# Optimization experiments

Hardware: AMD Instinct MI355X
Metric: run time of the kernel (lower is better)

## Reference

```python
import jax, jax.numpy as jnp
import numpy as np

B, T, L = 16, 32, 128
D = 768            # PhoBERT-base hidden size
NH = 12            # attn_num_heads
HD = D // NH
VOCAB = 64000
NEG = -1e9


def setup_inputs() -> dict:
    key = jax.random.key(0)
    ks = jax.random.split(key, 12)
    input_ids = jax.random.randint(ks[0], (B, T, L), 0, VOCAB, dtype=jnp.int32)
    attention_mask = jnp.ones((B, T, L), dtype=jnp.float32)
    # ragged number of real turns per dialogue
    num_turns = jax.random.randint(ks[1], (B,), 4, T + 1)
    turn_mask = (jnp.arange(T)[None, :] < num_turns[:, None]).astype(jnp.float32)
    s = 0.02
    embed = jax.random.normal(ks[2], (VOCAB, D), jnp.float32) * s
    Wq = jax.random.normal(ks[3], (D, D), jnp.float32) * s
    Wk = jax.random.normal(ks[4], (D, D), jnp.float32) * s
    Wv = jax.random.normal(ks[5], (D, D), jnp.float32) * s
    Wo = jax.random.normal(ks[6], (D, D), jnp.float32) * s
    bq = jnp.zeros((D,), jnp.float32)
    bk = jnp.zeros((D,), jnp.float32)
    bv = jnp.zeros((D,), jnp.float32)
    bo = jnp.zeros((D,), jnp.float32)
    Wh = jax.random.normal(ks[7], (2 * D,), jnp.float32) * s
    bh = jnp.zeros((), jnp.float32)
    return dict(input_ids=input_ids, attention_mask=attention_mask,
                turn_mask=turn_mask, embed=embed,
                Wq=Wq, bq=bq, Wk=Wk, bk=bk, Wv=Wv, bv=bv, Wo=Wo, bo=bo,
                Wh=Wh, bh=bh)


def _forward(input_ids, attention_mask, turn_mask, embed,
             Wq, bq, Wk, bk, Wv, bv, Wo, bo, Wh, bh):
    # --- turn encoder (frozen PhoBERT stand-in): embedding + masked mean pool ---
    emb = embed[input_ids]                                  # [B,T,L,D]
    m = attention_mask[..., None]                           # [B,T,L,1]
    H = (emb * m).sum(axis=2) / jnp.clip(m.sum(axis=2), 1.0)  # [B,T,D]

    # --- cross-turn attention: query = h_t, keys/values = H[:t] (strictly causal) ---
    q = (H @ Wq + bq).reshape(B, T, NH, HD)
    k = (H @ Wk + bk).reshape(B, T, NH, HD)
    v = (H @ Wv + bv).reshape(B, T, NH, HD)
    scores = jnp.einsum('bqhd,bkhd->bhqk', q, k) / np.sqrt(HD)  # [B,NH,T,T]
    idx = jnp.arange(T)
    strict = (idx[None, :, None] > idx[None, None, :])          # [1,T,T] j < i
    kmask = strict & (turn_mask[:, None, :] > 0)                # [B,T,T]
    scores = jnp.where(kmask[:, None, :, :], scores, NEG)
    attn = jax.nn.softmax(scores, axis=-1)
    ctx = jnp.einsum('bhqk,bkhd->bqhd', attn, v).reshape(B, T, D)
    ctx = ctx @ Wo + bo                                         # [B,T,D]
    # t == 0 uses c_t = zeros (no MHA output, no output bias)
    ctx = ctx * (idx > 0)[None, :, None]

    # --- evidence head + noisy-or recurrence ---
    z = jnp.concatenate([H, ctx], axis=-1)                      # [B,T,2D]
    s = z @ Wh + bh                                             # [B,T]
    qprob = jax.nn.sigmoid(s) * turn_mask                       # padded turns -> q=0
    one_minus = 1.0 - qprob
    p_agg = 1.0 - jnp.cumprod(one_minus, axis=1)                # [B,T]
    p_dialogue = 1.0 - jnp.prod(one_minus, axis=1)              # [B]
    return qprob, p_agg, p_dialogue


def reference(input_ids, attention_mask, turn_mask, embed,
              Wq, bq, Wk, bk, Wv, bv, Wo, bo, Wh, bh):
    return _forward(input_ids, attention_mask, turn_mask, embed,
                    Wq, bq, Wk, bk, Wv, bv, Wo, bo, Wh, bh)
```

## Files before the change

### kernel.cpp

```cpp
#include <hip/hip_runtime.h>
#include <hip/hip_bf16.h>
#include <math.h>

#define B_ 16
#define T_ 32
#define L_ 128
#define D_ 768
#define NH_ 12
#define HD_ 64
#define M_ (B_*T_)

typedef __attribute__((ext_vector_type(8))) short s16x8;
typedef __attribute__((ext_vector_type(4))) float f32x4;
typedef __attribute__((ext_vector_type(8))) unsigned short u16x8;

__device__ __forceinline__ unsigned short f2bf(float x) {
    unsigned int b = __float_as_uint(x);
    b += 0x7FFFu + ((b >> 16) & 1u);
    return (unsigned short)(b >> 16);
}

#define MFMA16(a, b, c) __builtin_amdgcn_mfma_f32_16x16x32_bf16(a, b, c, 0, 0, 0)

__global__ __launch_bounds__(384) void pool_prep_kernel(
    const int* __restrict__ ids, const float* __restrict__ amask,
    const float* __restrict__ embed,
    const float* __restrict__ Wq, const float* __restrict__ Wk,
    const float* __restrict__ Wv, const float* __restrict__ Wo,
    unsigned short* __restrict__ Wt, unsigned short* __restrict__ Wot,
    float* __restrict__ Ppart, float* __restrict__ PartM)
{
    const int bx  = blockIdx.x;
    const int tid = threadIdx.x;
    if (bx < M_*4) {
        const int bt = bx >> 2, l0 = (bx & 3) * 32;
        const int tx = tid % 96, ph = tid / 96;
        __shared__ int   sid[32];
        __shared__ float smk[32];
        __shared__ float red[4][96][9];
        if (tid < 32) {
            sid[tid] = ids[bt*L_ + l0 + tid];
            smk[tid] = amask[bt*L_ + l0 + tid];
        }
        __syncthreads();
        float a0=0,a1=0,a2=0,a3=0,a4=0,a5=0,a6=0,a7=0, msump=0.f;
        #pragma unroll 8
        for (int l = ph; l < 32; l += 4) {
            float m = smk[l];
            msump += m;
            const float4* p = (const float4*)(embed + (size_t)sid[l]*D_) + (tx << 1);
            float4 v0 = p[0], v1 = p[1];
            a0 = fmaf(v0.x, m, a0); a1 = fmaf(v0.y, m, a1);
            a2 = fmaf(v0.z, m, a2); a3 = fmaf(v0.w, m, a3);
            a4 = fmaf(v1.x, m, a4); a5 = fmaf(v1.y, m, a5);
            a6 = fmaf(v1.z, m, a6); a7 = fmaf(v1.w, m, a7);
        }
        float* rr = red[ph][tx];
        rr[0]=a0; rr[1]=a1; rr[2]=a2; rr[3]=a3; rr[4]=a4; rr[5]=a5; rr[6]=a6; rr[7]=a7;
        if (tx == 0) rr[8] = msump;
        __syncthreads();
        if (ph == 0) {
            float4 o0, o1;
            o0.x = red[0][tx][0]+red[1][tx][0]+red[2][tx][0]+red[3][tx][0];
            o0.y = red[0][tx][1]+red[1][tx][1]+red[2][tx][1]+red[3][tx][1];
            o0.z = red[0][tx][2]+red[1][tx][2]+red[2][tx][2]+red[3][tx][2];
            o0.w = red[0][tx][3]+red[1][tx][3]+red[2][tx][3]+red[3][tx][3];
            o1.x = red[0][tx][4]+red[1][tx][4]+red[2][tx][4]+red[3][tx][4];
            o1.y = red[0][tx][5]+red[1][tx][5]+red[2][tx][5]+red[3][tx][5];
            o1.z = red[0][tx][6]+red[1][tx][6]+red[2][tx][6]+red[3][tx][6];
            o1.w = red[0][tx][7]+red[1][tx][7]+red[2][tx][7]+red[3][tx][7];
            float* dst = Ppart + (size_t)bx*D_ + tx*8;
            *(float4*)dst = o0;
            *(float4*)(dst + 4) = o1;
            if (tx == 0)
                PartM[bx] = red[0][0][8]+red[1][0][8]+red[2][0][8]+red[3][0][8];
        }
    } else {
        const int idx = bx - M_*4;
        const int z   = idx / 384;
        const int rem = idx % 384;
        const int n0  = (rem % 16) * 48;
        const int k0  = (rem / 16) * 32;
        const float* __restrict__ W = (z==0)?Wq:(z==1)?Wk:(z==2)?Wv:Wo;
        unsigned short* __restrict__ outp = (z<3) ? (Wt + (size_t)z*D_*D_) : Wot;
        __shared__ float tile[32][49];
        {
            const int tx2 = tid % 48, ty2 = tid / 48;
            #pragma unroll
            for (int r = 0; r < 4; ++r)
                tile[ty2 + r*8][tx2] = W[(size_t)(k0 + ty2 + r*8)*D_ + n0 + tx2];
        }
        __syncthreads();
        {
            const int tk = tid % 32, tn = tid / 32;
            #pragma unroll
            for (int r = 0; r < 4; ++r)
                outp[(size_t)(n0 + tn + r*12)*D_ + k0 + tk] = f2bf(tile[tk][tn + r*12]);
        }
    }
}

__global__ __launch_bounds__(96) void combine_kernel(
    const float* __restrict__ Ppart, const float* __restrict__ PartM,
    const float* __restrict__ Wh,
    unsigned short* __restrict__ Hbf, float* __restrict__ s1)
{
    const int bt = blockIdx.x, tx = threadIdx.x;
    __shared__ float dp[96];
    float msum = PartM[bt*4] + PartM[bt*4+1] + PartM[bt*4+2] + PartM[bt*4+3];
    float inv = 1.f / fmaxf(msum, 1.f);
    const float* p0 = Ppart + (size_t)(bt*4)*D_ + tx*8;
    float s[8];
    #pragma unroll
    for (int k = 0; k < 8; ++k)
        s[k] = (p0[k] + p0[D_ + k] + p0[2*D_ + k] + p0[3*D_ + k]) * inv;
    u16x8 hb;
    #pragma unroll
    for (int k = 0; k < 8; ++k) hb[k] = f2bf(s[k]);
    *(u16x8*)(Hbf + (size_t)bt*D_ + tx*8) = hb;
    float d = 0.f;
    #pragma unroll
    for (int k = 0; k < 8; ++k) d = fmaf(s[k], Wh[tx*8 + k], d);
    dp[tx] = d;
    __syncthreads();
    if (tx < 32) {
        float dd = dp[tx] + dp[tx+32] + dp[tx+64];
        #pragma unroll
        for (int off = 16; off > 0; off >>= 1) dd += __shfl_xor(dd, off, 32);
        if (tx == 0) s1[bt] = dd;
    }
}

__global__ __launch_bounds__(256) void qkv_attn_kernel(
    const unsigned short* __restrict__ Hbf,
    const unsigned short* __restrict__ Wt,
    const float* __restrict__ bq, const float* __restrict__ bk, const float* __restrict__ bv,
    const float* __restrict__ tmask,
    unsigned short* __restrict__ ctx)
{
    const int b = blockIdx.x / NH_;
    const int h = blockIdx.x % NH_;
    const int tid  = threadIdx.x;
    const int lane = tid & 63;
    const int w    = tid >> 6;
    const int r16  = lane & 15;
    const int kgrp = lane >> 4;

    __shared__ unsigned short Hs[32][776];
    __shared__ unsigned short Qs[32][72];
    __shared__ unsigned short Ks[32][72];
    __shared__ unsigned short Vt[64][40];
    __shared__ unsigned short Ps[32][40];

    const unsigned short* hsrc = Hbf + (size_t)b*T_*D_;
    #pragma unroll
    for (int it = 0; it < 12; ++it) {
        int e = it*256 + tid;
        int row = e / 96, cg = e % 96;
        *(s16x8*)&Hs[row][cg*8] = *(const s16x8*)(hsrc + row*D_ + cg*8);
    }
    __syncthreads();

    const int nc = h*HD_ + w*16 + r16;
    const unsigned short* wq = Wt + (size_t)nc*D_;
    const unsigned short* wk = wq + (size_t)D_*D_;
    const unsigned short* wv = wk + (size_t)D_*D_;
    f32x4 aQ0={0,0,0,0},aQ1={0,0,0,0},aK0={0,0,0,0},aK1={0,0,0,0},aV0={0,0,0,0},aV1={0,0,0,0};
    s16x8 pq = *(const s16x8*)(wq + kgrp*8);
    s16x8 pk = *(const s16x8*)(wk + kgrp*8);
    s16x8 pv = *(const s16x8*)(wv + kgrp*8);
    for (int k0 = 0; k0 < D_; k0 += 32) {
        s16x8 cq = pq, ck = pk, cv = pv;
        int kn = k0 + 32;
        if (kn < D_) {
            pq = *(const s16x8*)(wq + kn + kgrp*8);
            pk = *(const s16x8*)(wk + kn + kgrp*8);
            pv = *(const s16x8*)(wv + kn + kgrp*8);
        }
        s16x8 a0 = *(const s16x8*)&Hs[r16][k0 + kgrp*8];
        s16x8 a1 = *(const s16x8*)&Hs[16 + r16][k0 + kgrp*8];
        aQ0 = MFMA16(a0, cq, aQ0); aQ1 = MFMA16(a1, cq, aQ1);
        aK0 = MFMA16(a0, ck, aK0); aK1 = MFMA16(a1, ck, aK1);
        aV0 = MFMA16(a0, cv, aV0); aV1 = MFMA16(a1, cv, aV1);
    }
    {
        const int c = w*16 + r16;
        const float bQ = bq[h*HD_ + c], bK = bk[h*HD_ + c], bV = bv[h*HD_ + c];
        #pragma unroll
        for (int mi = 0; mi < 2; ++mi) {
            f32x4 q_ = mi ? aQ1 : aQ0;
            f32x4 k_ = mi ? aK1 : aK0;
            f32x4 v_ = mi ? aV1 : aV0;
            #pragma unroll
            for (int r = 0; r < 4; ++r) {
                int i = mi*16 + kgrp*4 + r;
                Qs[i][c] = f2bf(q_[r] + bQ);
                Ks[i][c] = f2bf(k_[r] + bK);
                Vt[c][i] = f2bf(v_[r] + bV);
            }
        }
    }
    __syncthreads();

    f32x4 s00={0,0,0,0}, s01={0,0,0,0}, s10={0,0,0,0}, s11={0,0,0,0};
    #pragma unroll
    for (int ks = 0; ks < 2; ++ks) {
        s16x8 q0 = *(const s16x8*)&Qs[r16][ks*32 + kgrp*8];
        s16x8 q1 = *(const s16x8*)&Qs[16 + r16][ks*32 + kgrp*8];
        s16x8 k0v = *(const s16x8*)&Ks[r16][ks*32 + kgrp*8];
        s16x8 k1v = *(const s16x8*)&Ks[16 + r16][ks*32 + kgrp*8];
        s00 = MFMA16(q0, k0v, s00); s01 = MFMA16(q0, k1v, s01);
        s10 = MFMA16(q1, k0v, s10); s11 = MFMA16(q1, k1v, s11);
    }

    const float tmj0 = tmask[b*T_ + r16];
    const float tmj1 = tmask[b*T_ + 16 + r16];
    const int miW = w >> 1, niW = w & 1;
    #pragma unroll
    for (int mi = 0; mi < 2; ++mi) {
        f32x4 sv0 = mi ? s10 : s00;
        f32x4 sv1 = mi ? s11 : s01;
        #pragma unroll
        for (int r = 0; r < 4; ++r) {
            int i = mi*16 + kgrp*4 + r;
            float v0 = (r16 < i      && tmj0 > 0.f) ? sv0[r]*0.125f : -1e9f;
            float v1 = (16 + r16 < i && tmj1 > 0.f) ? sv1[r]*0.125f : -1e9f;
            float mx = fmaxf(v0, v1);
            #pragma unroll
            for (int off = 1; off < 16; off <<= 1) mx = fmaxf(mx, __shfl_xor(mx, off));
            float e0 = __expf(v0 - mx), e1 = __expf(v1 - mx);
            float sm = e0 + e1;
            #pragma unroll
            for (int off = 1; off < 16; off <<= 1) sm += __shfl_xor(sm, off);
            float inv = 1.f / sm;
            if (mi == miW) {
                float p = (niW ? e1 : e0) * inv;
                Ps[i][niW*16 + r16] = f2bf(p);
            }
        }
    }
    __syncthreads();

    {
        s16x8 ap0 = *(const s16x8*)&Ps[r16][kgrp*8];
        s16x8 ap1 = *(const s16x8*)&Ps[16 + r16][kgrp*8];
        s16x8 bvv = *(const s16x8*)&Vt[w*16 + r16][kgrp*8];
        f32x4 o0 = {0,0,0,0}, o1 = {0,0,0,0};
        o0 = MFMA16(ap0, bvv, o0);
        o1 = MFMA16(ap1, bvv, o1);
        #pragma unroll
        for (int mi = 0; mi < 2; ++mi) {
            f32x4 o_ = mi ? o1 : o0;
            #pragma unroll
            for (int r = 0; r < 4; ++r) {
                int i = mi*16 + kgrp*4 + r;
                ctx[(size_t)(b*T_ + i)*D_ + h*HD_ + w*16 + r16] = f2bf(o_[r]);
            }
        }
    }
}

__global__ __launch_bounds__(256) void gemm_head_kernel(
    const unsigned short* __restrict__ Abf,
    const unsigned short* __restrict__ Wtn,
    const float* __restrict__ bias,
    const float* __restrict__ Wh,
    float* __restrict__ s2p)
{
    const int bn = blockIdx.x;
    const int n0 = bn * 64;
    const int m0 = blockIdx.y * 64;

    __shared__ unsigned short As[64][40];
    __shared__ unsigned short Bs[64][40];
    __shared__ float s2l[64][2];

    const int tid  = threadIdx.x;
    const int lane = tid & 63;
    const int wave = tid >> 6;
    const int wm   = wave >> 1;
    const int wn   = wave & 1;
    const int kgrp = lane >> 4;
    const int r16  = lane & 15;

    const int srow = tid >> 2;
    const int scol = (tid & 3) * 8;

    f32x4 acc00 = {0,0,0,0}, acc01 = {0,0,0,0}, acc10 = {0,0,0,0}, acc11 = {0,0,0,0};

    for (int k0 = 0; k0 < D_; k0 += 32) {
        s16x8 av = *(const s16x8*)(Abf + (size_t)(m0 + srow)*D_ + k0 + scol);
        s16x8 bv = *(const s16x8*)(Wtn + (size_t)(n0 + srow)*D_ + k0 + scol);
        *(s16x8*)&As[srow][scol] = av;
        *(s16x8*)&Bs[srow][scol] = bv;
        __syncthreads();
        s16x8 a0 = *(const s16x8*)&As[wm*32 +      r16][kgrp*8];
        s16x8 a1 = *(const s16x8*)&As[wm*32 + 16 + r16][kgrp*8];
        s16x8 bb0 = *(const s16x8*)&Bs[wn*32 +      r16][kgrp*8];
        s16x8 bb1 = *(const s16x8*)&Bs[wn*32 + 16 + r16][kgrp*8];
        acc00 = MFMA16(a0, bb0, acc00);
        acc01 = MFMA16(a0, bb1, acc01);
        acc10 = MFMA16(a1, bb0, acc10);
        acc11 = MFMA16(a1, bb1, acc11);
        __syncthreads();
    }

    float rp[2][4] = {};
    #pragma unroll
    for (int ni = 0; ni < 2; ++ni) {
        int col = n0 + wn*32 + ni*16 + r16;
        float w2 = Wh[D_ + col];
        float bv_ = bias[col];
        #pragma unroll
        for (int mi = 0; mi < 2; ++mi) {
            f32x4 c = (mi == 0) ? (ni == 0 ? acc00 : acc01) : (ni == 0 ? acc10 : acc11);
            #pragma unroll
            for (int r = 0; r < 4; ++r) {
                int m = m0 + wm*32 + mi*16 + kgrp*4 + r;
                float v = c[r] + bv_;
                if ((m & (T_ - 1)) == 0) v = 0.f;
                rp[mi][r] = fmaf(v, w2, rp[mi][r]);
            }
        }
    }
    #pragma unroll
    for (int mi = 0; mi < 2; ++mi)
        #pragma unroll
        for (int r = 0; r < 4; ++r) {
            float v = rp[mi][r];
            v += __shfl_xor(v, 1); v += __shfl_xor(v, 2);
            v += __shfl_xor(v, 4); v += __shfl_xor(v, 8);
            rp[mi][r] = v;
        }
    if (r16 == 0) {
        #pragma unroll
        for (int mi = 0; mi < 2; ++mi)
            #pragma unroll
            for (int r = 0; r < 4; ++r)
                s2l[wm*32 + mi*16 + kgrp*4 + r][wn] = rp[mi][r];
    }
    __syncthreads();
    if (tid < 64)
        s2p[(size_t)(m0 + tid)*12 + bn] = s2l[tid][0] + s2l[tid][1];
}

__global__ __launch_bounds__(512) void scan_kernel(
    const float* __restrict__ s1, const float* __restrict__ s2p,
    const float* __restrict__ bh, const float* __restrict__ tmask,
    float* __restrict__ qprob, float* __restrict__ p_agg, float* __restrict__ p_dlg)
{
    const int bt = threadIdx.x;
    const int t  = bt & 31, b = bt >> 5;
    float s = s1[bt] + bh[0];
    #pragma unroll
    for (int c = 0; c < 12; ++c) s += s2p[bt*12 + c];
    float q = (1.f / (1.f + __expf(-s))) * tmask[bt];
    qprob[bt] = q;
    float x = 1.f - q;
    #pragma unroll
    for (int off = 1; off < 32; off <<= 1) {
        float y = __shfl_up(x, off, 32);
        if (t >= off) x *= y;
    }
    p_agg[bt] = 1.f - x;
    if (t == 31) p_dlg[b] = 1.f - x;
}

extern "C" void kernel_launch(void* const* d_in, const int* in_sizes, int n_in,
                              void* d_out, int out_size, void* d_ws, size_t ws_size,
                              hipStream_t stream) {
    const int*   ids   = (const int*)  d_in[0];
    const float* amask = (const float*)d_in[1];
    const float* tmask = (const float*)d_in[2];
    const float* embed = (const float*)d_in[3];
    const float* Wq    = (const float*)d_in[4];
    const float* bq    = (const float*)d_in[5];
    const float* Wk    = (const float*)d_in[6];
    const float* bk    = (const float*)d_in[7];
    const float* Wv    = (const float*)d_in[8];
    const float* bv    = (const float*)d_in[9];
    const float* Wo    = (const float*)d_in[10];
    const float* bo    = (const float*)d_in[11];
    const float* Wh    = (const float*)d_in[12];
    const float* bh    = (const float*)d_in[13];
    float* out = (float*)d_out;

    unsigned short* Hbf   = (unsigned short*)d_ws;
    unsigned short* CTXbf = Hbf + (size_t)M_*D_;
    unsigned short* Wt    = CTXbf + (size_t)M_*D_;
    unsigned short* Wot   = Wt + (size_t)3*D_*D_;
    float* s1    = (float*)(Wot + (size_t)D_*D_);
    float* s2p   = s1 + M_;
    float* PartM = s2p + M_*12;
    float* Ppart = PartM + M_*4;

    pool_prep_kernel<<<M_*4 + 1536, 384, 0, stream>>>(
        ids, amask, embed, Wq, Wk, Wv, Wo, Wt, Wot, Ppart, PartM);
    combine_kernel<<<M_, 96, 0, stream>>>(Ppart, PartM, Wh, Hbf, s1);
    qkv_attn_kernel<<<B_*NH_, 256, 0, stream>>>(Hbf, Wt, bq, bk, bv, tmask, CTXbf);
    gemm_head_kernel<<<dim3(12, 8), 256, 0, stream>>>(CTXbf, Wot, bo, Wh, s2p);
    scan_kernel<<<1, 512, 0, stream>>>(s1, s2p, bh, tmask, out, out + M_, out + 2*M_);
}
```

Measured before the change: 66.85 us.

## Fuse pool/combine and gemm/scan kernels, prefetch GEMM tiles into registers

The pooling kernel now processes a whole turn per block, computing the mean, the bf16 H and the first head dot product in one pass. This removes the separate combine kernel and the partial-sum buffers. The scan is folded into the output GEMM through a last-block-done atomic counter per row tile, which removes another launch. The GEMM also prefetches the next K slice into registers while the current one is consumed. In exchange, the pooling stage has fewer, longer blocks (512 instead of 2048), which may reduce parallelism on the gather.

```diff
diff --git a/kernel.cpp b/kernel.cpp
--- a/kernel.cpp
+++ b/kernel.cpp
@@ -27,25 +27,30 @@
     const float* __restrict__ embed,
     const float* __restrict__ Wq, const float* __restrict__ Wk,
     const float* __restrict__ Wv, const float* __restrict__ Wo,
+    const float* __restrict__ Wh,
     unsigned short* __restrict__ Wt, unsigned short* __restrict__ Wot,
-    float* __restrict__ Ppart, float* __restrict__ PartM)
+    unsigned short* __restrict__ Hbf, float* __restrict__ s1,
+    int* __restrict__ cnt)
 {
     const int bx  = blockIdx.x;
     const int tid = threadIdx.x;
-    if (bx < M_*4) {
-        const int bt = bx >> 2, l0 = (bx & 3) * 32;
+    if (bx < M_) {
+        const int bt = bx;
         const int tx = tid % 96, ph = tid / 96;
-        __shared__ int   sid[32];
-        __shared__ float smk[32];
+        __shared__ int   sid[L_];
+        __shared__ float smk[L_];
         __shared__ float red[4][96][9];
-        if (tid < 32) {
-            sid[tid] = ids[bt*L_ + l0 + tid];
-            smk[tid] = amask[bt*L_ + l0 + tid];
+        __shared__ float dp[96];
+        if (tid < L_) {
+            sid[tid] = ids[bt*L_ + tid];
+            smk[tid] = amask[bt*L_ + tid];
+        } else if (bx == 0 && tid < L_ + 8) {
+            cnt[tid - L_] = 0;
         }
         __syncthreads();
         float a0=0,a1=0,a2=0,a3=0,a4=0,a5=0,a6=0,a7=0, msump=0.f;
         #pragma unroll 8
-        for (int l = ph; l < 32; l += 4) {
+        for (int l = ph; l < L_; l += 4) {
             float m = smk[l];
             msump += m;
             const float4* p = (const float4*)(embed + (size_t)sid[l]*D_) + (tx << 1);
@@ -60,23 +65,30 @@
         if (tx == 0) rr[8] = msump;
         __syncthreads();
         if (ph == 0) {
-            float4 o0, o1;
-            o0.x = red[0][tx][0]+red[1][tx][0]+red[2][tx][0]+red[3][tx][0];
-            o0.y = red[0][tx][1]+red[1][tx][1]+red[2][tx][1]+red[3][tx][1];
-            o0.z = red[0][tx][2]+red[1][tx][2]+red[2][tx][2]+red[3][tx][2];
-            o0.w = red[0][tx][3]+red[1][tx][3]+red[2][tx][3]+red[3][tx][3];
-            o1.x = red[0][tx][4]+red[1][tx][4]+red[2][tx][4]+red[3][tx][4];
-            o1.y = red[0][tx][5]+red[1][tx][5]+red[2][tx][5]+red[3][tx][5];
-            o1.z = red[0][tx][6]+red[1][tx][6]+red[2][tx][6]+red[3][tx][6];
-            o1.w = red[0][tx][7]+red[1][tx][7]+red[2][tx][7]+red[3][tx][7];
-            float* dst = Ppart + (size_t)bx*D_ + tx*8;
-            *(float4*)dst = o0;
-            *(float4*)(dst + 4) = o1;
-            if (tx == 0)
-                PartM[bx] = red[0][0][8]+red[1][0][8]+red[2][0][8]+red[3][0][8];
+            float msum = red[0][0][8]+red[1][0][8]+red[2][0][8]+red[3][0][8];
+            float inv = 1.f / fmaxf(msum, 1.f);
+            float s[8];
+            u16x8 hb;
+            #pragma unroll
+            for (int k = 0; k < 8; ++k) {
+                s[k] = (red[0][tx][k]+red[1][tx][k]+red[2][tx][k]+red[3][tx][k]) * inv;
+                hb[k] = f2bf(s[k]);
+            }
+            *(u16x8*)(Hbf + (size_t)bt*D_ + tx*8) = hb;
+            float d = 0.f;
+            #pragma unroll
+            for (int k = 0; k < 8; ++k) d = fmaf(s[k], Wh[tx*8 + k], d);
+            dp[tx] = d;
+        }
+        __syncthreads();
+        if (tid < 32) {
+            float dd = dp[tid] + dp[tid+32] + dp[tid+64];
+            #pragma unroll
+            for (int off = 16; off > 0; off >>= 1) dd += __shfl_xor(dd, off, 32);
+            if (tid == 0) s1[bt] = dd;
         }
     } else {
-        const int idx = bx - M_*4;
+        const int idx = bx - M_;
         const int z   = idx / 384;
         const int rem = idx % 384;
         const int n0  = (rem % 16) * 48;
@@ -97,37 +109,6 @@
             for (int r = 0; r < 4; ++r)
                 outp[(size_t)(n0 + tn + r*12)*D_ + k0 + tk] = f2bf(tile[tk][tn + r*12]);
         }
-    }
-}
-
-__global__ __launch_bounds__(96) void combine_kernel(
-    const float* __restrict__ Ppart, const float* __restrict__ PartM,
-    const float* __restrict__ Wh,
-    unsigned short* __restrict__ Hbf, float* __restrict__ s1)
-{
-    const int bt = blockIdx.x, tx = threadIdx.x;
-    __shared__ float dp[96];
-    float msum = PartM[bt*4] + PartM[bt*4+1] + PartM[bt*4+2] + PartM[bt*4+3];
-    float inv = 1.f / fmaxf(msum, 1.f);
-    const float* p0 = Ppart + (size_t)(bt*4)*D_ + tx*8;
-    float s[8];
-    #pragma unroll
-    for (int k = 0; k < 8; ++k)
-        s[k] = (p0[k] + p0[D_ + k] + p0[2*D_ + k] + p0[3*D_ + k]) * inv;
-    u16x8 hb;
-    #pragma unroll
-    for (int k = 0; k < 8; ++k) hb[k] = f2bf(s[k]);
-    *(u16x8*)(Hbf + (size_t)bt*D_ + tx*8) = hb;
-    float d = 0.f;
-    #pragma unroll
-    for (int k = 0; k < 8; ++k) d = fmaf(s[k], Wh[tx*8 + k], d);
-    dp[tx] = d;
-    __syncthreads();
-    if (tx < 32) {
-        float dd = dp[tx] + dp[tx+32] + dp[tx+64];
-        #pragma unroll
-        for (int off = 16; off > 0; off >>= 1) dd += __shfl_xor(dd, off, 32);
-        if (tx == 0) s1[bt] = dd;
     }
 }
 
@@ -260,12 +241,17 @@
     }
 }
 
-__global__ __launch_bounds__(256) void gemm_head_kernel(
+__global__ __launch_bounds__(256) void gemm_head_scan_kernel(
     const unsigned short* __restrict__ Abf,
     const unsigned short* __restrict__ Wtn,
     const float* __restrict__ bias,
     const float* __restrict__ Wh,
-    float* __restrict__ s2p)
+    const float* __restrict__ s1,
+    const float* __restrict__ bh,
+    const float* __restrict__ tmask,
+    int* __restrict__ cnt,
+    float* __restrict__ s2p,
+    float* __restrict__ qprob, float* __restrict__ p_agg, float* __restrict__ p_dlg)
 {
     const int bn = blockIdx.x;
     const int n0 = bn * 64;
@@ -274,6 +260,7 @@
     __shared__ unsigned short As[64][40];
     __shared__ unsigned short Bs[64][40];
     __shared__ float s2l[64][2];
+    __shared__ int sdone;
 
     const int tid  = threadIdx.x;
     const int lane = tid & 63;
@@ -288,12 +275,19 @@
 
     f32x4 acc00 = {0,0,0,0}, acc01 = {0,0,0,0}, acc10 = {0,0,0,0}, acc11 = {0,0,0,0};
 
+    const unsigned short* aptr = Abf + (size_t)(m0 + srow)*D_ + scol;
+    const unsigned short* bptr = Wtn + (size_t)(n0 + srow)*D_ + scol;
+    s16x8 av = *(const s16x8*)aptr;
+    s16x8 bv2 = *(const s16x8*)bptr;
+
     for (int k0 = 0; k0 < D_; k0 += 32) {
-        s16x8 av = *(const s16x8*)(Abf + (size_t)(m0 + srow)*D_ + k0 + scol);
-        s16x8 bv = *(const s16x8*)(Wtn + (size_t)(n0 + srow)*D_ + k0 + scol);
         *(s16x8*)&As[srow][scol] = av;
-        *(s16x8*)&Bs[srow][scol] = bv;
-        __syncthreads();
+        *(s16x8*)&Bs[srow][scol] = bv2;
+        __syncthreads();
+        if (k0 + 32 < D_) {
+            av  = *(const s16x8*)(aptr + k0 + 32);
+            bv2 = *(const s16x8*)(bptr + k0 + 32);
+        }
         s16x8 a0 = *(const s16x8*)&As[wm*32 +      r16][kgrp*8];
         s16x8 a1 = *(const s16x8*)&As[wm*32 + 16 + r16][kgrp*8];
         s16x8 bb0 = *(const s16x8*)&Bs[wn*32 +      r16][kgrp*8];
@@ -342,28 +336,32 @@
     __syncthreads();
     if (tid < 64)
         s2p[(size_t)(m0 + tid)*12 + bn] = s2l[tid][0] + s2l[tid][1];
-}
-
-__global__ __launch_bounds__(512) void scan_kernel(
-    const float* __restrict__ s1, const float* __restrict__ s2p,
-    const float* __restrict__ bh, const float* __restrict__ tmask,
-    float* __restrict__ qprob, float* __restrict__ p_agg, float* __restrict__ p_dlg)
-{
-    const int bt = threadIdx.x;
-    const int t  = bt & 31, b = bt >> 5;
-    float s = s1[bt] + bh[0];
-    #pragma unroll
-    for (int c = 0; c < 12; ++c) s += s2p[bt*12 + c];
-    float q = (1.f / (1.f + __expf(-s))) * tmask[bt];
-    qprob[bt] = q;
-    float x = 1.f - q;
-    #pragma unroll
-    for (int off = 1; off < 32; off <<= 1) {
-        float y = __shfl_up(x, off, 32);
-        if (t >= off) x *= y;
-    }
-    p_agg[bt] = 1.f - x;
-    if (t == 31) p_dlg[b] = 1.f - x;
+
+    __threadfence();
+    __syncthreads();
+    if (tid == 0)
+        sdone = (atomicAdd(cnt + blockIdx.y, 1) == 11) ? 1 : 0;
+    __syncthreads();
+    if (sdone) {
+        __threadfence();
+        if (tid < 64) {
+            const int m = m0 + tid;
+            float s = s1[m] + bh[0];
+            #pragma unroll
+            for (int c = 0; c < 12; ++c) s += s2p[(size_t)m*12 + c];
+            float q = (1.f / (1.f + __expf(-s))) * tmask[m];
+            qprob[m] = q;
+            float x = 1.f - q;
+            const int t = tid & 31;
+            #pragma unroll
+            for (int off = 1; off < 32; off <<= 1) {
+                float y = __shfl_up(x, off, 32);
+                if (t >= off) x *= y;
+            }
+            p_agg[m] = 1.f - x;
+            if (t == 31) p_dlg[m >> 5] = 1.f - x;
+        }
+    }
 }
 
 extern "C" void kernel_launch(void* const* d_in, const int* in_sizes, int n_in,
@@ -389,15 +387,13 @@
     unsigned short* CTXbf = Hbf + (size_t)M_*D_;
     unsigned short* Wt    = CTXbf + (size_t)M_*D_;
     unsigned short* Wot   = Wt + (size_t)3*D_*D_;
-    float* s1    = (float*)(Wot + (size_t)D_*D_);
-    float* s2p   = s1 + M_;
-    float* PartM = s2p + M_*12;
-    float* Ppart = PartM + M_*4;
-
-    pool_prep_kernel<<<M_*4 + 1536, 384, 0, stream>>>(
-        ids, amask, embed, Wq, Wk, Wv, Wo, Wt, Wot, Ppart, PartM);
-    combine_kernel<<<M_, 96, 0, stream>>>(Ppart, PartM, Wh, Hbf, s1);
+    float* s1  = (float*)(Wot + (size_t)D_*D_);
+    float* s2p = s1 + M_;
+    int*   cnt = (int*)(s2p + (size_t)M_*12);
+
+    pool_prep_kernel<<<M_ + 1536, 384, 0, stream>>>(
+        ids, amask, embed, Wq, Wk, Wv, Wo, Wh, Wt, Wot, Hbf, s1, cnt);
     qkv_attn_kernel<<<B_*NH_, 256, 0, stream>>>(Hbf, Wt, bq, bk, bv, tmask, CTXbf);
-    gemm_head_kernel<<<dim3(12, 8), 256, 0, stream>>>(CTXbf, Wot, bo, Wh, s2p);
-    scan_kernel<<<1, 512, 0, stream>>>(s1, s2p, bh, tmask, out, out + M_, out + 2*M_);
-}
+    gemm_head_scan_kernel<<<dim3(12, 8), 256, 0, stream>>>(
+        CTXbf, Wot, bo, Wh, s1, bh, tmask, cnt, s2p, out, out + M_, out + 2*M_);
+}
```

After: 71.72 us. 7.3% more time.
